# Kernel optimization log

Measured on AMD Instinct MI355X. Metric: run time of the kernel, lower is better.

The kernel has to match this reference:

```python
import jax, jax.numpy as jnp
import numpy as np

DIM = 128
HID = 1024
B = 1024


def _mlp(x, W1, b1, W2, b2, W3, b3):
    h = jnp.tanh(x @ W1 + b1)
    h = jnp.tanh(h @ W2 + b2)
    return h @ W3 + b3


def setup_inputs() -> dict:
    key = jax.random.key(0)
    ks = jax.random.split(key, 8)

    def w(k, shape):
        return (jax.random.normal(k, shape, jnp.float32) / np.float32(np.sqrt(shape[0])))

    # states = [mu | sigma_diag]; sigma_diag must be positive (it is a variance)
    states = jax.random.uniform(ks[0], (B, 2 * DIM), jnp.float32) + jnp.float32(0.05)
    t = jnp.float32(0.25)
    inp = dict(states=states, t=t)
    # dynamics_net params (input = dim + 1 for time)
    inp["dW1"] = w(ks[1], (DIM + 1, HID)); inp["db1"] = jnp.zeros((HID,), jnp.float32)
    inp["dW2"] = w(ks[2], (HID, HID));     inp["db2"] = jnp.zeros((HID,), jnp.float32)
    inp["dW3"] = w(ks[3], (HID, DIM));     inp["db3"] = jnp.zeros((DIM,), jnp.float32)
    # noise_net params (diagonal Q via softplus)
    inp["nW1"] = w(ks[4], (DIM + 1, HID)); inp["nb1"] = jnp.zeros((HID,), jnp.float32)
    inp["nW2"] = w(ks[5], (HID, HID));     inp["nb2"] = jnp.zeros((HID,), jnp.float32)
    inp["nW3"] = w(ks[6], (HID, DIM));     inp["nb3"] = jnp.zeros((DIM,), jnp.float32)
    return inp


def reference(states, t, dW1, db1, dW2, db2, dW3, db3, nW1, nb1, nW2, nb2, nW3, nb3):
    dim = DIM
    mu = states[:, :dim]          # [B, dim]
    sigma = states[:, dim:]       # [B, dim] diagonal covariance
    tcol = jnp.full((mu.shape[0], 1), t, mu.dtype)

    # drift of the mean (batched MLP)
    mu_drift = _mlp(jnp.concatenate([mu, tcol], axis=1), dW1, db1, dW2, db2, dW3, db3)

    # diagonal of the Jacobian d mu_drift / d mu, per sample.
    # The torch code loops over dim doing one autograd.grad per row; here one
    # vmapped jacfwd collapses that into a single batched forward-mode pass.
    def dyn_single(mu_s):  # [dim] -> [dim]
        x = jnp.concatenate([mu_s, jnp.reshape(t, (1,))])
        return _mlp(x, dW1, db1, dW2, db2, dW3, db3)

    J = jax.vmap(jax.jacfwd(dyn_single))(mu)          # [B, dim, dim]
    J_diag = jnp.diagonal(J, axis1=1, axis2=2)         # [B, dim]

    # process noise: diagonal of Q (softplus for PSD)
    q_raw = _mlp(jnp.concatenate([mu, tcol], axis=1), nW1, nb1, nW2, nb2, nW3, nb3)
    Q_diag = jax.nn.softplus(q_raw)                    # [B, dim]

    sigma_drift = 2.0 * J_diag * sigma + Q_diag
    log_density_drift = -jnp.sum(J_diag, axis=1) + 0.5 * jnp.sum(
        Q_diag / (sigma + 1e-6), axis=1
    )
    return jnp.concatenate([mu_drift, sigma_drift], axis=1), log_density_drift
```

## Files before the change

kernel.cpp:

```cpp
#include <hip/hip_runtime.h>
#include <math.h>

typedef unsigned short u16;
typedef unsigned int u32;
typedef __bf16 bf16x8 __attribute__((ext_vector_type(8)));
typedef float f32x4 __attribute__((ext_vector_type(4)));

#define NB 1024
#define HID 1024

__device__ __forceinline__ float bfu(u16 u) { return __uint_as_float(((u32)u) << 16); }
__device__ __forceinline__ u16 f2bf(float f) {
    u32 u = __float_as_uint(f);
    return (u16)((u + 0x7fffu + ((u >> 16) & 1u)) >> 16);
}
__device__ __forceinline__ u32 mulbf2(u32 a, u32 b) {
    float a0 = __uint_as_float(a << 16), a1 = __uint_as_float(a & 0xffff0000u);
    float b0 = __uint_as_float(b << 16), b1 = __uint_as_float(b & 0xffff0000u);
    u32 u0 = __float_as_uint(a0 * b0), u1 = __float_as_uint(a1 * b1);
    return ((u0 + 0x8000u) >> 16) | ((u1 + 0x8000u) & 0xffff0000u);
}

#if __has_builtin(__builtin_amdgcn_global_load_lds)
#define HAVE_GLL 1
#else
#define HAVE_GLL 0
#endif

__device__ __forceinline__ void stage16(const void* g, void* ldsbase, int lane) {
#if HAVE_GLL
    typedef const __attribute__((address_space(1))) unsigned char ga_t;
    typedef __attribute__((address_space(3))) unsigned char la_t;
    __builtin_amdgcn_global_load_lds((ga_t*)(unsigned long long)g,
                                     (la_t*)(u32)(unsigned long long)ldsbase,
                                     16, 0, 0);
#else
    *reinterpret_cast<uint4*>((char*)ldsbase + lane * 16) =
        *reinterpret_cast<const uint4*>(g);
#endif
}

#define SBAR __builtin_amdgcn_sched_barrier(0)


__device__ __forceinline__ void stage_tile(const u16* src, int ld, u16* dst, int tid) {
    int w = tid >> 6, lane = tid & 63;
#pragma unroll
    for (int q = 0; q < 4; ++q) {
        int rbase = q * 32 + w * 8;
        int row = rbase + (lane >> 3);
        stage16(src + (size_t)row * ld + (lane & 7) * 8, dst + rbase * 64, lane);
    }
}

__device__ __forceinline__ void mfma_block(const u16* As, const u16* Bs,
                                           f32x4 acc[4][4], int wr, int wc, int lane) {
    int lr = lane >> 4, lc = lane & 15;
#pragma unroll
    for (int kc = 0; kc < 64; kc += 32) {
        bf16x8 av[4], bv[4];
#pragma unroll
        for (int it = 0; it < 4; ++it)
            av[it] = *(const bf16x8*)&As[(wr * 64 + it * 16 + lc) * 64 + kc + lr * 8];
#pragma unroll
        for (int nt = 0; nt < 4; ++nt)
            bv[nt] = *(const bf16x8*)&Bs[(wc * 64 + nt * 16 + lc) * 64 + kc + lr * 8];
#pragma unroll
        for (int it = 0; it < 4; ++it)
#pragma unroll
            for (int nt = 0; nt < 4; ++nt)
                acc[it][nt] = __builtin_amdgcn_mfma_f32_16x16x32_bf16(
                    av[it], bv[nt], acc[it][nt], 0, 0, 0);
    }
}


__global__ __launch_bounds__(256) void k_cast(const float* in, u16* out, int n) {
    int i = blockIdx.x * 256 + threadIdx.x;
    if (i < n) out[i] = f2bf(in[i]);
}

__global__ __launch_bounds__(256) void k_transposeB(const float* inA, const float* inB,
                                                    u16* outA, u16* outB, int R, int C) {
    const float* in = blockIdx.z ? inB : inA;
    u16* out = blockIdx.z ? outB : outA;
    __shared__ u16 tile[32][33];
    int c0 = blockIdx.x * 32, r0 = blockIdx.y * 32;
    int tx = threadIdx.x, ty = threadIdx.y;
#pragma unroll
    for (int dy = 0; dy < 32; dy += 8)
        tile[ty + dy][tx] = f2bf(in[(size_t)(r0 + ty + dy) * C + c0 + tx]);
    __syncthreads();
#pragma unroll
    for (int dy = 0; dy < 32; dy += 8)
        out[(size_t)(c0 + ty + dy) * R + r0 + tx] = tile[tx][ty + dy];
}

__global__ __launch_bounds__(256) void k_layer1(const float* states, const float* tptr,
                                                const float* dW1, const float* db1,
                                                const float* nW1, const float* nb1,
                                                u16* h1d, u16* h1n, u16* g1d) {
    __shared__ float xt[129][8];
    int blk = blockIdx.x, q = blockIdx.y, net = blockIdx.z, tid = threadIdx.x;
    float t = *tptr;
    for (int idx = tid; idx < 8 * 128; idx += 256) {
        int d = idx >> 3, s = idx & 7;
        xt[d][s] = states[(size_t)(blk * 8 + s) * 256 + d];
    }
    if (tid < 8) xt[128][tid] = t;
    __syncthreads();
    const float* W = net ? nW1 : dW1;
    const float* bi = net ? nb1 : db1;
    u16* H = net ? h1n : h1d;
    int o = q * 256 + tid;
    float acc[8] = {0.f, 0.f, 0.f, 0.f, 0.f, 0.f, 0.f, 0.f};
    for (int d = 0; d < 129; ++d) {
        float w = W[(size_t)d * 1024 + o];
        float4 xa = *(const float4*)&xt[d][0];
        float4 xb = *(const float4*)&xt[d][4];
        acc[0] += xa.x * w; acc[1] += xa.y * w; acc[2] += xa.z * w; acc[3] += xa.w * w;
        acc[4] += xb.x * w; acc[5] += xb.y * w; acc[6] += xb.z * w; acc[7] += xb.w * w;
    }
    float b = bi[o];
#pragma unroll
    for (int s = 0; s < 8; ++s) {
        float h = tanhf(acc[s] + b);
        H[(size_t)(blk * 8 + s) * 1024 + o] = f2bf(h);
        if (!net) g1d[(size_t)(blk * 8 + s) * 1024 + o] = f2bf(1.f - h * h);
    }
}

__global__ __launch_bounds__(256) void k_l2part(const u16* Ad, const u16* An,
                                                const u16* Wd, const u16* Wn,
                                                float* P) {
    int x = blockIdx.x;
    int nt = x & 7, ks = x >> 3;
    int mt = blockIdx.y, net = blockIdx.z;
    const u16* A = net ? An : Ad;
    const u16* W = net ? Wn : Wd;
    int n0 = nt * 128, row0 = mt * 128;
    int kbeg = ks * 512;
    __shared__ __align__(16) u16 As[128 * 64], Bs[128 * 64];
    int tid = threadIdx.x, w = tid >> 6, lane = tid & 63;
    int wr = w >> 1, wc = w & 1, lr = lane >> 4, lc = lane & 15;
    f32x4 acc[4][4];
#pragma unroll
    for (int a = 0; a < 4; ++a)
#pragma unroll
        for (int b2 = 0; b2 < 4; ++b2) { f32x4 zz = {0.f, 0.f, 0.f, 0.f}; acc[a][b2] = zz; }
    for (int k0 = kbeg; k0 < kbeg + 512; k0 += 64) {
        stage_tile(A + (size_t)row0 * 1024 + k0, 1024, As, tid);
        stage_tile(W + (size_t)n0 * 1024 + k0, 1024, Bs, tid);
        __syncthreads();
        mfma_block(As, Bs, acc, wr, wc, lane);
        __syncthreads();
    }
    float* dst = P + (size_t)(net * 2 + ks) * 1024 * 1024;
#pragma unroll
    for (int it = 0; it < 4; ++it)
#pragma unroll
        for (int nt2 = 0; nt2 < 4; ++nt2) {
            int col = n0 + wc * 64 + nt2 * 16 + lc;
#pragma unroll
            for (int r = 0; r < 4; ++r) {
                int row = row0 + wr * 64 + it * 16 + lr * 4 + r;
                dst[(size_t)row * 1024 + col] = acc[it][nt2][r];
            }
        }
}

__global__ __launch_bounds__(256) void k_h2fin(const float* P, const float* db2,
                                               const float* nb2, u16* h2d, u16* h2n) {
    int net = blockIdx.y;
    const float* b = net ? nb2 : db2;
    u16* H = net ? h2n : h2d;
    size_t idx = (size_t)blockIdx.x * 256 + threadIdx.x;
    int col = (int)(idx & 1023);
    const float* P0 = P + (size_t)(net * 2) * 1024 * 1024;
    const float* P1 = P + (size_t)(net * 2 + 1) * 1024 * 1024;
    H[idx] = f2bf(tanhf(P0[idx] + P1[idx] + b[col]));
}

__global__ __launch_bounds__(256) void k_l3part(const u16* Ad, const u16* An,
                                                const u16* Wd, const u16* Wn,
                                                float* P) {
    int ks = blockIdx.x, mt = blockIdx.y, net = blockIdx.z;
    const u16* A = net ? An : Ad;
    const u16* W = net ? Wn : Wd;
    int row0 = mt * 128, kbeg = ks * 256;
    __shared__ __align__(16) u16 As[128 * 64], Bs[128 * 64];
    int tid = threadIdx.x, w = tid >> 6, lane = tid & 63;
    int wr = w >> 1, wc = w & 1, lr = lane >> 4, lc = lane & 15;
    f32x4 acc[4][4];
#pragma unroll
    for (int a = 0; a < 4; ++a)
#pragma unroll
        for (int b2 = 0; b2 < 4; ++b2) { f32x4 zz = {0.f, 0.f, 0.f, 0.f}; acc[a][b2] = zz; }
    for (int k0 = kbeg; k0 < kbeg + 256; k0 += 64) {
        stage_tile(A + (size_t)row0 * 1024 + k0, 1024, As, tid);
        stage_tile(W + (size_t)k0, 1024, Bs, tid);
        __syncthreads();
        mfma_block(As, Bs, acc, wr, wc, lane);
        __syncthreads();
    }
    float* dst = P + (size_t)(net * 4 + ks) * 1024 * 128;
#pragma unroll
    for (int it = 0; it < 4; ++it)
#pragma unroll
        for (int nt2 = 0; nt2 < 4; ++nt2) {
            int col = wc * 64 + nt2 * 16 + lc;
#pragma unroll
            for (int r = 0; r < 4; ++r) {
                int row = row0 + wr * 64 + it * 16 + lr * 4 + r;
                dst[(size_t)row * 128 + col] = acc[it][nt2][r];
            }
        }
}


__device__ __forceinline__ void stage256(const u16* panel, int k0, u16* dst, int tid) {
    int lane = tid & 63, w = tid >> 6;
#pragma unroll
    for (int q = 0; q < 4; ++q) {
        int Dhalf = q * 4096 + w * 512 + lane * 8;
        int row = Dhalf >> 6;
        int chunk = (Dhalf >> 3) & 7;
        int src_chunk = chunk ^ (row & 7);
        stage16(panel + (size_t)row * 1024 + k0 + src_chunk * 8,
                dst + q * 4096 + w * 512, lane);
    }
}

struct ARegs { uint4 wv[4]; uint4 gv[4]; };

__device__ __forceinline__ void issueA(const u16* dW1bf, const u16* g1d, int mt,
                                       int k0, int tid, ARegs& ar) {
#pragma unroll
    for (int q = 0; q < 4; ++q) {
        int cid = q * 512 + tid;
        int r = cid >> 3, c = cid & 7;
        ar.wv[q] = *(const uint4*)&dW1bf[(size_t)(r & 127) * 1024 + k0 + c * 8];
        ar.gv[q] = *(const uint4*)&g1d[(size_t)(2 * mt + (r >> 7)) * 1024 + k0 + c * 8];
    }
}

__device__ __forceinline__ void writeA(u16* As_, int tid, const ARegs& ar) {
#pragma unroll
    for (int q = 0; q < 4; ++q) {
        int cid = q * 512 + tid;
        int r = cid >> 3, c = cid & 7;
        uint4 o;
        o.x = mulbf2(ar.wv[q].x, ar.gv[q].x);
        o.y = mulbf2(ar.wv[q].y, ar.gv[q].y);
        o.z = mulbf2(ar.wv[q].z, ar.gv[q].z);
        o.w = mulbf2(ar.wv[q].w, ar.gv[q].w);
        *(uint4*)&As_[r * 64 + ((c ^ (r & 7)) << 3)] = o;
    }
}

__device__ __forceinline__ void compute256(const u16* As, const u16* Bs,
                                           f32x4 acc[8][4], int wr, int wc, int lane) {
    int lr = lane >> 4, lc = lane & 15;
#pragma unroll
    for (int kh = 0; kh < 2; ++kh) {
        bf16x8 av[8], bv[4];
#pragma unroll
        for (int m = 0; m < 8; ++m) {
            int row = wr * 128 + m * 16 + lc;
            int chunk = (kh * 4 + lr) ^ (row & 7);
            av[m] = *(const bf16x8*)&As[row * 64 + chunk * 8];
        }
#pragma unroll
        for (int n = 0; n < 4; ++n) {
            int row = wc * 64 + n * 16 + lc;
            int chunk = (kh * 4 + lr) ^ (row & 7);
            bv[n] = *(const bf16x8*)&Bs[row * 64 + chunk * 8];
        }
#pragma unroll
        for (int m = 0; m < 8; ++m)
#pragma unroll
            for (int n = 0; n < 4; ++n)
                acc[m][n] = __builtin_amdgcn_mfma_f32_16x16x32_bf16(
                    av[m], bv[n], acc[m][n], 0, 0, 0);
    }
}

__global__ __launch_bounds__(512, 2) void k_jacf(const u16* dW1bf, const u16* g1d,
                                                 const u16* W2T, const u16* W3T,
                                                 const u16* h2d, float* Jpart) {
    __shared__ __align__(16) u16 smem[2][2][16384];
    int tid = threadIdx.x, lane = tid & 63, w = tid >> 6;
    int wr = w >> 2, wc = w & 3, lr = lane >> 4, lc = lane & 15;
    int hID = blockIdx.x;
    int lin = (hID & 7) * 256 + (hID >> 3);
    int mt = lin >> 2, nt = lin & 3;
    int n0 = nt * 256;
    const u16* Bp = W2T + (size_t)n0 * 1024;

    f32x4 acc[8][4];
#pragma unroll
    for (int m = 0; m < 8; ++m)
#pragma unroll
        for (int n = 0; n < 4; ++n) { f32x4 zz = {0.f, 0.f, 0.f, 0.f}; acc[m][n] = zz; }

    ARegs ar;
    issueA(dW1bf, g1d, mt, 0, tid, ar);
    stage256(Bp, 0, &smem[0][1][0], tid);
    writeA(&smem[0][0][0], tid, ar);
    __syncthreads();

    for (int t = 0; t < 16; ++t) {
        int p = t & 1;
        if (t < 15) {
            issueA(dW1bf, g1d, mt, (t + 1) * 64, tid, ar);
            stage256(Bp, (t + 1) * 64, &smem[p ^ 1][1][0], tid);
        }
        SBAR;
        __builtin_amdgcn_s_setprio(1);
        compute256(&smem[p][0][0], &smem[p][1][0], acc, wr, wc, lane);
        __builtin_amdgcn_s_setprio(0);
        if (t < 15) writeA(&smem[p ^ 1][0][0], tid, ar);
        __syncthreads();
    }

    int b = 2 * mt + wr;
    float g2v[4];
#pragma unroll
    for (int n = 0; n < 4; ++n) {
        int k2 = n0 + wc * 64 + n * 16 + lc;
        float h2 = bfu(h2d[(size_t)b * 1024 + k2]);
        g2v[n] = 1.f - h2 * h2;
    }
    float* jtmp = (float*)&smem[0][0][0];
#pragma unroll
    for (int m = 0; m < 8; ++m) {
#pragma unroll
        for (int r = 0; r < 4; ++r) {
            int i = m * 16 + lr * 4 + r;
            float p = 0.f;
#pragma unroll
            for (int n = 0; n < 4; ++n) {
                int k2 = n0 + wc * 64 + n * 16 + lc;
                float w3 = bfu(W3T[(size_t)i * 1024 + k2]);
                p += acc[m][n][r] * g2v[n] * w3;
            }
#pragma unroll
            for (int msk = 1; msk < 16; msk <<= 1) p += __shfl_xor(p, msk, 64);
            if (lc == 0) jtmp[wc * 256 + wr * 128 + i] = p;
        }
    }
    __syncthreads();
    if (tid < 256) {
        float s = jtmp[tid] + jtmp[256 + tid] + jtmp[512 + tid] + jtmp[768 + tid];
        int bb = 2 * mt + (tid >> 7);
        Jpart[((size_t)bb * 4 + nt) * 128 + (tid & 127)] = s;
    }
}

__global__ __launch_bounds__(128) void k_final(const float* states, const float* Jpart,
                                               const float* L3part, const float* db3,
                                               const float* nb3, float* out) {
    int b = blockIdx.x, i = threadIdx.x;
    float jd = 0.f;
#pragma unroll
    for (int kb = 0; kb < 4; ++kb) jd += Jpart[((size_t)b * 4 + kb) * 128 + i];
    float mu = db3[i], qr = nb3[i];
#pragma unroll
    for (int ks = 0; ks < 4; ++ks) {
        mu += L3part[((size_t)(0 * 4 + ks) * 1024 + b) * 128 + i];
        qr += L3part[((size_t)(1 * 4 + ks) * 1024 + b) * 128 + i];
    }
    out[(size_t)b * 256 + i] = mu;
    float q = (qr > 20.f) ? qr : log1pf(expf(qr));
    float sig = states[(size_t)b * 256 + 128 + i];
    out[(size_t)b * 256 + 128 + i] = 2.f * jd * sig + q;
    float s1 = jd;
    float s2 = q / (sig + 1e-6f);
#pragma unroll
    for (int m = 32; m >= 1; m >>= 1) {
        s1 += __shfl_down(s1, m, 64);
        s2 += __shfl_down(s2, m, 64);
    }
    __shared__ float red[4];
    int wv = i >> 6, ln = i & 63;
    if (ln == 0) { red[wv * 2] = s1; red[wv * 2 + 1] = s2; }
    __syncthreads();
    if (i == 0) out[(size_t)NB * 256 + b] = -(red[0] + red[2]) + 0.5f * (red[1] + red[3]);
}

extern "C" void kernel_launch(void* const* d_in, const int* in_sizes, int n_in,
                              void* d_out, int out_size, void* d_ws, size_t ws_size,
                              hipStream_t stream) {
    (void)in_sizes; (void)n_in; (void)out_size; (void)ws_size;
    const float* states = (const float*)d_in[0];
    const float* tptr   = (const float*)d_in[1];
    const float* dW1 = (const float*)d_in[2];  const float* db1 = (const float*)d_in[3];
    const float* dW2 = (const float*)d_in[4];  const float* db2 = (const float*)d_in[5];
    const float* dW3 = (const float*)d_in[6];  const float* db3 = (const float*)d_in[7];
    const float* nW1 = (const float*)d_in[8];  const float* nb1 = (const float*)d_in[9];
    const float* nW2 = (const float*)d_in[10]; const float* nb2 = (const float*)d_in[11];
    const float* nW3 = (const float*)d_in[12]; const float* nb3 = (const float*)d_in[13];
    float* out = (float*)d_out;
    char* ws = (char*)d_ws;

    u16* dW1bf = (u16*)(ws + 0);
    u16* dW2T  = (u16*)(ws + 262144);
    u16* nW2T  = (u16*)(ws + 2359296);
    u16* dW3T  = (u16*)(ws + 4456448);
    u16* nW3T  = (u16*)(ws + 4718592);
    u16* h1d   = (u16*)(ws + 4980736);
    u16* h1n   = (u16*)(ws + 7077888);
    u16* h2d   = (u16*)(ws + 9175040);
    u16* h2n   = (u16*)(ws + 11272192);
    u16* g1d   = (u16*)(ws + 13369344);
    float* Jpart  = (float*)(ws + 15466496);
    float* L3part = (float*)(ws + 17563648);
    float* H2part = (float*)(ws + 21757952);

    k_cast<<<512, 256, 0, stream>>>(dW1, dW1bf, 128 * 1024);
    dim3 tb(32, 8);
    k_transposeB<<<dim3(32, 32, 2), tb, 0, stream>>>(dW2, nW2, dW2T, nW2T, 1024, 1024);
    k_transposeB<<<dim3(4, 32, 2), tb, 0, stream>>>(dW3, nW3, dW3T, nW3T, 1024, 128);
    k_layer1<<<dim3(128, 4, 2), 256, 0, stream>>>(states, tptr, dW1, db1, nW1, nb1,
                                                  h1d, h1n, g1d);
    k_l2part<<<dim3(16, 8, 2), 256, 0, stream>>>(h1d, h1n, dW2T, nW2T, H2part);
    k_h2fin<<<dim3(4096, 2), 256, 0, stream>>>(H2part, db2, nb2, h2d, h2n);
    k_l3part<<<dim3(4, 8, 2), 256, 0, stream>>>(h2d, h2n, dW3T, nW3T, L3part);
    k_jacf<<<2048, 512, 0, stream>>>(dW1bf, g1d, dW2T, dW3T, h2d, Jpart);
    k_final<<<1024, 128, 0, stream>>>(states, Jpart, L3part, db3, nb3, out);
}
```

Baseline: 388.2 us.

## Split Jacobian GEMM main loop into four interleaved LDS-read/MFMA phases

```diff
diff --git a/kernel.cpp b/kernel.cpp
--- a/kernel.cpp
+++ b/kernel.cpp
@@ -41,6 +41,9 @@
 }
 
 #define SBAR __builtin_amdgcn_sched_barrier(0)
+#define WBAR __builtin_amdgcn_s_barrier()
+#define LKW0 asm volatile("s_waitcnt lgkmcnt(0)" ::: "memory")
+#define VW0  asm volatile("s_waitcnt vmcnt(0)" ::: "memory")
 
 
 __device__ __forceinline__ void stage_tile(const u16* src, int ld, u16* dst, int tid) {
@@ -218,10 +221,12 @@
 }
 
 
-__device__ __forceinline__ void stage256(const u16* panel, int k0, u16* dst, int tid) {
+__device__ __forceinline__ void stage256h(const u16* panel, int k0, int h,
+                                          u16* dst, int tid) {
     int lane = tid & 63, w = tid >> 6;
 #pragma unroll
-    for (int q = 0; q < 4; ++q) {
+    for (int qq = 0; qq < 2; ++qq) {
+        int q = h * 2 + qq;
         int Dhalf = q * 4096 + w * 512 + lane * 8;
         int row = Dhalf >> 6;
         int chunk = (Dhalf >> 3) & 7;
@@ -258,31 +263,71 @@
     }
 }
 
-__device__ __forceinline__ void compute256(const u16* As, const u16* Bs,
-                                           f32x4 acc[8][4], int wr, int wc, int lane) {
-    int lr = lane >> 4, lc = lane & 15;
-#pragma unroll
-    for (int kh = 0; kh < 2; ++kh) {
-        bf16x8 av[8], bv[4];
-#pragma unroll
-        for (int m = 0; m < 8; ++m) {
-            int row = wr * 128 + m * 16 + lc;
-            int chunk = (kh * 4 + lr) ^ (row & 7);
-            av[m] = *(const bf16x8*)&As[row * 64 + chunk * 8];
-        }
-#pragma unroll
-        for (int n = 0; n < 4; ++n) {
-            int row = wc * 64 + n * 16 + lc;
-            int chunk = (kh * 4 + lr) ^ (row & 7);
-            bv[n] = *(const bf16x8*)&Bs[row * 64 + chunk * 8];
-        }
-#pragma unroll
-        for (int m = 0; m < 8; ++m)
-#pragma unroll
-            for (int n = 0; n < 4; ++n)
-                acc[m][n] = __builtin_amdgcn_mfma_f32_16x16x32_bf16(
-                    av[m], bv[n], acc[m][n], 0, 0, 0);
-    }
+__device__ __forceinline__ bf16x8 rdA(const u16* T, int wr, int m, int lc, int kq) {
+    int row = wr * 128 + m * 16 + lc;
+    return *(const bf16x8*)&T[row * 64 + ((kq ^ (row & 7)) << 3)];
+}
+__device__ __forceinline__ bf16x8 rdB(const u16* T, int wc, int n, int lc, int kq) {
+    int row = wc * 64 + n * 16 + lc;
+    return *(const bf16x8*)&T[row * 64 + ((kq ^ (row & 7)) << 3)];
+}
+
+#define MFMA16(AV, B0, B1, N0, N1)                                          \
+    __builtin_amdgcn_s_setprio(1);                                          \
+    _Pragma("unroll")                                                       \
+    for (int m_ = 0; m_ < 8; ++m_) {                                        \
+        acc[m_][N0] = __builtin_amdgcn_mfma_f32_16x16x32_bf16(AV[m_], B0,   \
+                                                              acc[m_][N0], 0, 0, 0); \
+        acc[m_][N1] = __builtin_amdgcn_mfma_f32_16x16x32_bf16(AV[m_], B1,   \
+                                                              acc[m_][N1], 0, 0, 0); \
+    }                                                                       \
+    __builtin_amdgcn_s_setprio(0);
+
+template <bool STG>
+__device__ __forceinline__ void jacf_iter(int t, u16 (*smem)[2][16384],
+                                          const u16* dW1bf, const u16* g1d,
+                                          const u16* Bp, int mt,
+                                          f32x4 (&acc)[8][4], ARegs& ar, int tid,
+                                          int wr, int wc, int lr, int lc) {
+    int p = t & 1, pn = p ^ 1;
+    const u16* As_ = &smem[p][0][0];
+    const u16* Bs_ = &smem[p][1][0];
+    bf16x8 avA[8], avB[8], bv0, bv1;
+
+#pragma unroll
+    for (int m = 0; m < 8; ++m) avA[m] = rdA(As_, wr, m, lc, lr);
+    bv0 = rdB(Bs_, wc, 0, lc, lr);
+    bv1 = rdB(Bs_, wc, 1, lc, lr);
+    if (STG) stage256h(Bp, (t + 1) * 64, 0, &smem[pn][1][0], tid);
+    SBAR; WBAR; LKW0; SBAR;
+    MFMA16(avA, bv0, bv1, 0, 1);
+    SBAR; WBAR; SBAR;
+
+    bv0 = rdB(Bs_, wc, 2, lc, lr);
+    bv1 = rdB(Bs_, wc, 3, lc, lr);
+#pragma unroll
+    for (int m = 0; m < 8; ++m) avB[m] = rdA(As_, wr, m, lc, 4 + lr);
+    if (STG) stage256h(Bp, (t + 1) * 64, 1, &smem[pn][1][0], tid);
+    SBAR; WBAR; LKW0; SBAR;
+    MFMA16(avA, bv0, bv1, 2, 3);
+    SBAR; WBAR; SBAR;
+
+    bv0 = rdB(Bs_, wc, 0, lc, 4 + lr);
+    bv1 = rdB(Bs_, wc, 1, lc, 4 + lr);
+    if (STG) issueA(dW1bf, g1d, mt, (t + 1) * 64, tid, ar);
+    SBAR; WBAR; LKW0; SBAR;
+    MFMA16(avB, bv0, bv1, 0, 1);
+    SBAR; WBAR; SBAR;
+
+    bv0 = rdB(Bs_, wc, 2, lc, 4 + lr);
+    bv1 = rdB(Bs_, wc, 3, lc, 4 + lr);
+    SBAR; WBAR; LKW0; SBAR;
+    MFMA16(avB, bv0, bv1, 2, 3);
+    SBAR;
+    if (STG) writeA(&smem[pn][0][0], tid, ar);
+    VW0;
+    LKW0;
+    SBAR; WBAR; SBAR;
 }
 
 __global__ __launch_bounds__(512, 2) void k_jacf(const u16* dW1bf, const u16* g1d,
@@ -305,23 +350,14 @@
 
     ARegs ar;
     issueA(dW1bf, g1d, mt, 0, tid, ar);
-    stage256(Bp, 0, &smem[0][1][0], tid);
+    stage256h(Bp, 0, 0, &smem[0][1][0], tid);
+    stage256h(Bp, 0, 1, &smem[0][1][0], tid);
     writeA(&smem[0][0][0], tid, ar);
-    __syncthreads();
-
-    for (int t = 0; t < 16; ++t) {
-        int p = t & 1;
-        if (t < 15) {
-            issueA(dW1bf, g1d, mt, (t + 1) * 64, tid, ar);
-            stage256(Bp, (t + 1) * 64, &smem[p ^ 1][1][0], tid);
-        }
-        SBAR;
-        __builtin_amdgcn_s_setprio(1);
-        compute256(&smem[p][0][0], &smem[p][1][0], acc, wr, wc, lane);
-        __builtin_amdgcn_s_setprio(0);
-        if (t < 15) writeA(&smem[p ^ 1][0][0], tid, ar);
-        __syncthreads();
-    }
+    VW0; LKW0; SBAR; WBAR; SBAR;
+
+    for (int t = 0; t < 15; ++t)
+        jacf_iter<true>(t, smem, dW1bf, g1d, Bp, mt, acc, ar, tid, wr, wc, lr, lc);
+    jacf_iter<false>(15, smem, dW1bf, g1d, Bp, mt, acc, ar, tid, wr, wc, lr, lc);
 
     int b = 2 * mt + wr;
     float g2v[4];
```

Result: slower. 453.8 us (+16.9%).

## Shrink Jacobian GEMM tile to one sample per block with smaller K step

Applied to the files above, without the earlier changes.

```diff
diff --git a/kernel.cpp b/kernel.cpp
--- a/kernel.cpp
+++ b/kernel.cpp
@@ -218,125 +218,103 @@
 }
 
 
-__device__ __forceinline__ void stage256(const u16* panel, int k0, u16* dst, int tid) {
-    int lane = tid & 63, w = tid >> 6;
-#pragma unroll
-    for (int q = 0; q < 4; ++q) {
-        int Dhalf = q * 4096 + w * 512 + lane * 8;
-        int row = Dhalf >> 6;
-        int chunk = (Dhalf >> 3) & 7;
-        int src_chunk = chunk ^ (row & 7);
-        stage16(panel + (size_t)row * 1024 + k0 + src_chunk * 8,
-                dst + q * 4096 + w * 512, lane);
-    }
-}
-
-struct ARegs { uint4 wv[4]; uint4 gv[4]; };
-
-__device__ __forceinline__ void issueA(const u16* dW1bf, const u16* g1d, int mt,
-                                       int k0, int tid, ARegs& ar) {
-#pragma unroll
-    for (int q = 0; q < 4; ++q) {
-        int cid = q * 512 + tid;
-        int r = cid >> 3, c = cid & 7;
-        ar.wv[q] = *(const uint4*)&dW1bf[(size_t)(r & 127) * 1024 + k0 + c * 8];
-        ar.gv[q] = *(const uint4*)&g1d[(size_t)(2 * mt + (r >> 7)) * 1024 + k0 + c * 8];
-    }
-}
-
-__device__ __forceinline__ void writeA(u16* As_, int tid, const ARegs& ar) {
-#pragma unroll
-    for (int q = 0; q < 4; ++q) {
-        int cid = q * 512 + tid;
-        int r = cid >> 3, c = cid & 7;
+__global__ __launch_bounds__(512, 4) void k_jacf(const u16* dW1bf, const u16* g1d,
+                                                 const u16* W2T, const u16* W3T,
+                                                 const u16* h2d, float* Jpart) {
+    __shared__ __align__(16) u16 smA[2][128 * 32];
+    __shared__ __align__(16) u16 smB[2][256 * 32];
+    int tid = threadIdx.x, lane = tid & 63, w = tid >> 6;
+    int wr = w >> 2, wc = w & 3, lr = lane >> 4, lc = lane & 15;
+    int hID = blockIdx.x;
+    int lin = (hID & 7) * 512 + (hID >> 3);
+    int mt = lin >> 2, nt = lin & 3;
+    int n0 = nt * 256;
+    const u16* Bp = W2T + (size_t)n0 * 1024;
+    const u16* grow = g1d + (size_t)mt * 1024;
+
+    f32x4 acc[4][4];
+#pragma unroll
+    for (int m = 0; m < 4; ++m)
+#pragma unroll
+        for (int n = 0; n < 4; ++n) { f32x4 zz = {0.f, 0.f, 0.f, 0.f}; acc[m][n] = zz; }
+
+    int ar_ = tid >> 2, ac_ = tid & 3;
+    int asw = ac_ ^ ((ar_ >> 1) & 3);
+    uint4 wv, gv;
+
+    auto issueA = [&](int k0) {
+        wv = *(const uint4*)&dW1bf[(size_t)ar_ * 1024 + k0 + asw * 8];
+        gv = *(const uint4*)&grow[k0 + asw * 8];
+    };
+    auto writeA = [&](u16* dst) {
         uint4 o;
-        o.x = mulbf2(ar.wv[q].x, ar.gv[q].x);
-        o.y = mulbf2(ar.wv[q].y, ar.gv[q].y);
-        o.z = mulbf2(ar.wv[q].z, ar.gv[q].z);
-        o.w = mulbf2(ar.wv[q].w, ar.gv[q].w);
-        *(uint4*)&As_[r * 64 + ((c ^ (r & 7)) << 3)] = o;
-    }
-}
-
-__device__ __forceinline__ void compute256(const u16* As, const u16* Bs,
-                                           f32x4 acc[8][4], int wr, int wc, int lane) {
-    int lr = lane >> 4, lc = lane & 15;
-#pragma unroll
-    for (int kh = 0; kh < 2; ++kh) {
-        bf16x8 av[8], bv[4];
-#pragma unroll
-        for (int m = 0; m < 8; ++m) {
-            int row = wr * 128 + m * 16 + lc;
-            int chunk = (kh * 4 + lr) ^ (row & 7);
-            av[m] = *(const bf16x8*)&As[row * 64 + chunk * 8];
+        o.x = mulbf2(wv.x, gv.x);
+        o.y = mulbf2(wv.y, gv.y);
+        o.z = mulbf2(wv.z, gv.z);
+        o.w = mulbf2(wv.w, gv.w);
+        *(uint4*)&dst[ar_ * 32 + ac_ * 8] = o;
+    };
+    auto stageB = [&](int k0, u16* dst) {
+#pragma unroll
+        for (int q = 0; q < 2; ++q) {
+            int cid = q * 512 + tid;
+            int r = cid >> 2, c = cid & 3;
+            stage16(Bp + (size_t)r * 1024 + k0 + ((c ^ ((r >> 1) & 3)) << 3),
+                    dst + (q * 512 + w * 64) * 8, lane);
+        }
+    };
+    auto compute = [&](const u16* As_, const u16* Bs_) {
+        bf16x8 av[4], bv[4];
+#pragma unroll
+        for (int m = 0; m < 4; ++m) {
+            int row = wr * 64 + m * 16 + lc;
+            av[m] = *(const bf16x8*)&As_[row * 32 + ((lr ^ ((row >> 1) & 3)) << 3)];
         }
 #pragma unroll
         for (int n = 0; n < 4; ++n) {
             int row = wc * 64 + n * 16 + lc;
-            int chunk = (kh * 4 + lr) ^ (row & 7);
-            bv[n] = *(const bf16x8*)&Bs[row * 64 + chunk * 8];
-        }
-#pragma unroll
-        for (int m = 0; m < 8; ++m)
+            bv[n] = *(const bf16x8*)&Bs_[row * 32 + ((lr ^ ((row >> 1) & 3)) << 3)];
+        }
+        __builtin_amdgcn_s_setprio(1);
+#pragma unroll
+        for (int m = 0; m < 4; ++m)
 #pragma unroll
             for (int n = 0; n < 4; ++n)
                 acc[m][n] = __builtin_amdgcn_mfma_f32_16x16x32_bf16(
                     av[m], bv[n], acc[m][n], 0, 0, 0);
-    }
-}
-
-__global__ __launch_bounds__(512, 2) void k_jacf(const u16* dW1bf, const u16* g1d,
-                                                 const u16* W2T, const u16* W3T,
-                                                 const u16* h2d, float* Jpart) {
-    __shared__ __align__(16) u16 smem[2][2][16384];
-    int tid = threadIdx.x, lane = tid & 63, w = tid >> 6;
-    int wr = w >> 2, wc = w & 3, lr = lane >> 4, lc = lane & 15;
-    int hID = blockIdx.x;
-    int lin = (hID & 7) * 256 + (hID >> 3);
-    int mt = lin >> 2, nt = lin & 3;
-    int n0 = nt * 256;
-    const u16* Bp = W2T + (size_t)n0 * 1024;
-
-    f32x4 acc[8][4];
-#pragma unroll
-    for (int m = 0; m < 8; ++m)
-#pragma unroll
-        for (int n = 0; n < 4; ++n) { f32x4 zz = {0.f, 0.f, 0.f, 0.f}; acc[m][n] = zz; }
-
-    ARegs ar;
-    issueA(dW1bf, g1d, mt, 0, tid, ar);
-    stage256(Bp, 0, &smem[0][1][0], tid);
-    writeA(&smem[0][0][0], tid, ar);
+        __builtin_amdgcn_s_setprio(0);
+    };
+
+    issueA(0);
+    stageB(0, smB[0]);
+    writeA(smA[0]);
     __syncthreads();
 
-    for (int t = 0; t < 16; ++t) {
+    for (int t = 0; t < 32; ++t) {
         int p = t & 1;
-        if (t < 15) {
-            issueA(dW1bf, g1d, mt, (t + 1) * 64, tid, ar);
-            stage256(Bp, (t + 1) * 64, &smem[p ^ 1][1][0], tid);
+        if (t < 31) {
+            issueA((t + 1) * 32);
+            stageB((t + 1) * 32, smB[p ^ 1]);
         }
         SBAR;
-        __builtin_amdgcn_s_setprio(1);
-        compute256(&smem[p][0][0], &smem[p][1][0], acc, wr, wc, lane);
-        __builtin_amdgcn_s_setprio(0);
-        if (t < 15) writeA(&smem[p ^ 1][0][0], tid, ar);
+        compute(smA[p], smB[p]);
+        if (t < 31) writeA(smA[p ^ 1]);
         __syncthreads();
     }
 
-    int b = 2 * mt + wr;
     float g2v[4];
 #pragma unroll
     for (int n = 0; n < 4; ++n) {
         int k2 = n0 + wc * 64 + n * 16 + lc;
-        float h2 = bfu(h2d[(size_t)b * 1024 + k2]);
+        float h2 = bfu(h2d[(size_t)mt * 1024 + k2]);
         g2v[n] = 1.f - h2 * h2;
     }
-    float* jtmp = (float*)&smem[0][0][0];
-#pragma unroll
-    for (int m = 0; m < 8; ++m) {
+    float* jtmp = (float*)&smA[0][0];
+#pragma unroll
+    for (int m = 0; m < 4; ++m) {
 #pragma unroll
         for (int r = 0; r < 4; ++r) {
-            int i = m * 16 + lr * 4 + r;
+            int i = wr * 64 + m * 16 + lr * 4 + r;
             float p = 0.f;
 #pragma unroll
             for (int n = 0; n < 4; ++n) {
@@ -346,14 +324,13 @@
             }
 #pragma unroll
             for (int msk = 1; msk < 16; msk <<= 1) p += __shfl_xor(p, msk, 64);
-            if (lc == 0) jtmp[wc * 256 + wr * 128 + i] = p;
+            if (lc == 0) jtmp[wc * 128 + i] = p;
         }
     }
     __syncthreads();
-    if (tid < 256) {
-        float s = jtmp[tid] + jtmp[256 + tid] + jtmp[512 + tid] + jtmp[768 + tid];
-        int bb = 2 * mt + (tid >> 7);
-        Jpart[((size_t)bb * 4 + nt) * 128 + (tid & 127)] = s;
+    if (tid < 128) {
+        float s = jtmp[tid] + jtmp[128 + tid] + jtmp[256 + tid] + jtmp[384 + tid];
+        Jpart[((size_t)mt * 4 + nt) * 128 + tid] = s;
     }
 }
 
@@ -426,6 +403,6 @@
     k_l2part<<<dim3(16, 8, 2), 256, 0, stream>>>(h1d, h1n, dW2T, nW2T, H2part);
     k_h2fin<<<dim3(4096, 2), 256, 0, stream>>>(H2part, db2, nb2, h2d, h2n);
     k_l3part<<<dim3(4, 8, 2), 256, 0, stream>>>(h2d, h2n, dW3T, nW3T, L3part);
-    k_jacf<<<2048, 512, 0, stream>>>(dW1bf, g1d, dW2T, dW3T, h2d, Jpart);
+    k_jacf<<<4096, 512, 0, stream>>>(dW1bf, g1d, dW2T, dW3T, h2d, Jpart);
     k_final<<<1024, 128, 0, stream>>>(states, Jpart, L3part, db3, nb3, out);
 }
```

After: 381.7 us. About the same (-1.7%).
